# Optimization experiments

Hardware: AMD Instinct MI355X
Metric: run time of the kernel (lower is better)

The kernel has to match this reference:

```python
import jax, jax.numpy as jnp
import numpy as np

DT = 0.01
NJ = 7  # panda: 7 revolute joints, serial chain, fixed base
G_ACC = 9.81


def skew(v):
    x, y, z = v[..., 0], v[..., 1], v[..., 2]
    O = jnp.zeros_like(x)
    return jnp.stack([jnp.stack([O, -z, y], -1),
                      jnp.stack([z, O, -x], -1),
                      jnp.stack([-y, x, O], -1)], -2)


def rodrigues(axis, q):
    # axis [3], q [B] -> [B,3,3]
    K = skew(axis)
    K2 = K @ K
    s = jnp.sin(q)[:, None, None]
    c = jnp.cos(q)[:, None, None]
    return jnp.eye(3, dtype=q.dtype) + s * K + (1.0 - c) * K2


def xmot(E, r, v):
    # motion transform child<-parent; E [B,3,3], r [3], v [B,6] ([w;u] ordering)
    w, u = v[:, :3], v[:, 3:]
    wn = jnp.einsum('bij,bj->bi', E, w)
    un = jnp.einsum('bij,bj->bi', E, u - jnp.cross(jnp.broadcast_to(r, u.shape), w))
    return jnp.concatenate([wn, un], -1)


def crm(v, m):
    # motion cross product v x m
    w, u = v[:, :3], v[:, 3:]
    return jnp.concatenate([jnp.cross(w, m[:, :3]),
                            jnp.cross(w, m[:, 3:]) + jnp.cross(u, m[:, :3])], -1)


def crf(v, f):
    # force cross product v x* f
    w, u = v[:, :3], v[:, 3:]
    n, ff = f[:, :3], f[:, 3:]
    return jnp.concatenate([jnp.cross(w, n) + jnp.cross(u, ff), jnp.cross(w, ff)], -1)


def spatial_inertia(mass, com, inertia):
    # [NJ] / [NJ,3] / [NJ,3,3] -> [NJ,6,6] in [w;v] ordering
    cx = skew(com)
    m = mass[:, None, None]
    top = jnp.concatenate([inertia + m * (cx @ jnp.swapaxes(cx, -1, -2)), m * cx], -1)
    bot = jnp.concatenate([m * jnp.swapaxes(cx, -1, -2),
                           m * jnp.broadcast_to(jnp.eye(3, dtype=mass.dtype), cx.shape)], -1)
    return jnp.concatenate([top, bot], -2)


def aba(q, qd, tau, axes, R_fix, p_fix, mass, com, inertia):
    B = q.shape[0]
    I6 = spatial_inertia(mass, com, inertia)  # [NJ,6,6]
    E_l, S_l, v_l, c_l, IA_l, pA_l = [], [], [], [], [], []
    v_prev = None
    # pass 1: kinematics + bias terms
    for i in range(NJ):
        Rw = jnp.einsum('ij,bjk->bik', R_fix[i], rodrigues(axes[i], q[:, i]))
        E = jnp.swapaxes(Rw, -1, -2)  # parent->child rotation
        S = jnp.concatenate([axes[i], jnp.zeros(3, dtype=q.dtype)])  # [6]
        vJ = qd[:, i:i + 1] * S
        v_i = vJ if i == 0 else xmot(E, p_fix[i], v_prev) + vJ
        c_i = crm(v_i, vJ)
        Iv = jnp.einsum('ij,bj->bi', I6[i], v_i)
        pA_i = crf(v_i, Iv)
        E_l.append(E); S_l.append(S); v_l.append(v_i); c_l.append(c_i)
        IA_l.append(jnp.broadcast_to(I6[i], (B, 6, 6)))
        pA_l.append(pA_i)
        v_prev = v_i
    # pass 2: articulated inertia backward sweep
    U_l = [None] * NJ; d_l = [None] * NJ; uu_l = [None] * NJ
    for i in reversed(range(NJ)):
        S = S_l[i]; IA = IA_l[i]
        U = jnp.einsum('bij,j->bi', IA, S)
        d = jnp.einsum('bi,i->b', U, S)
        uu = tau[:, i] - jnp.einsum('bi,i->b', pA_l[i], S)
        U_l[i], d_l[i], uu_l[i] = U, d, uu
        if i > 0:
            Ia = IA - U[:, :, None] * U[:, None, :] / d[:, None, None]
            pa = pA_l[i] + jnp.einsum('bij,bj->bi', Ia, c_l[i]) + U * (uu / d)[:, None]
            E = E_l[i]; rX = skew(p_fix[i])
            Z = jnp.zeros_like(E)
            Xm = jnp.concatenate([jnp.concatenate([E, Z], -1),
                                  jnp.concatenate([-jnp.einsum('bij,jk->bik', E, rX), E], -1)], -2)
            IA_l[i - 1] = IA_l[i - 1] + jnp.einsum('bji,bjk,bkl->bil', Xm, Ia, Xm)
            fE = jnp.einsum('bji,bj->bi', E, pa[:, 3:])
            nP = jnp.einsum('bji,bj->bi', E, pa[:, :3]) + jnp.cross(jnp.broadcast_to(p_fix[i], fE.shape), fE)
            pA_l[i - 1] = pA_l[i - 1] + jnp.concatenate([nP, fE], -1)
    # pass 3: accelerations (base spatial accel = -gravity)
    a_prev = jnp.broadcast_to(jnp.array([0, 0, 0, 0, 0, G_ACC], dtype=q.dtype), (B, 6))
    qdd = []
    for i in range(NJ):
        ap = xmot(E_l[i], p_fix[i], a_prev) + c_l[i]
        qdd_i = (uu_l[i] - jnp.einsum('bi,bi->b', U_l[i], ap)) / d_l[i]
        a_prev = ap + qdd_i[:, None] * S_l[i]
        qdd.append(qdd_i)
    return jnp.stack(qdd, -1)  # [B,NJ]


def _rx(a):
    c, s = np.cos(a), np.sin(a)
    return np.array([[1, 0, 0], [0, c, -s], [0, s, c]], np.float32)


def setup_inputs() -> dict:
    key = jax.random.key(0)
    k1, k2 = jax.random.split(key)
    B = 262144
    x = 0.5 * jax.random.normal(k1, (B, 2 * NJ), dtype=jnp.float32)
    u = 5.0 * jax.random.normal(k2, (B, NJ), dtype=jnp.float32)
    angles = [0.0, -np.pi / 2, np.pi / 2, np.pi / 2, -np.pi / 2, np.pi / 2, np.pi / 2]
    R_fix = jnp.asarray(np.stack([_rx(a) for a in angles]).astype(np.float32))
    p_fix = jnp.asarray(np.array([[0, 0, 0.333], [0, 0, 0], [0, -0.316, 0], [0.0825, 0, 0],
                                  [-0.0825, 0.384, 0], [0, 0, 0], [0.088, 0, 0]], np.float32))
    axes = jnp.asarray(np.tile(np.array([0, 0, 1], np.float32), (NJ, 1)))
    mass = jnp.asarray(np.array([4.97, 0.65, 3.23, 3.59, 1.23, 1.67, 0.735], np.float32))
    com = jnp.asarray(np.array([[0.003, 0.002, -0.06], [-0.003, -0.028, 0.003], [0.027, 0.039, -0.066],
                                [-0.053, 0.104, 0.027], [-0.012, 0.041, -0.038], [0.06, -0.014, -0.011],
                                [0.01, -0.004, 0.061]], np.float32))
    diags = np.array([[0.7, 0.7, 0.01], [0.008, 0.028, 0.025], [0.037, 0.036, 0.011],
                      [0.026, 0.028, 0.031], [0.036, 0.036, 0.011], [0.002, 0.004, 0.005],
                      [0.012, 0.010, 0.005]], np.float32)
    inertia = jnp.asarray(np.stack([np.diag(v) for v in diags]).astype(np.float32))
    return {"x": x, "u": u, "axes": axes, "R_fix": R_fix, "p_fix": p_fix,
            "mass": mass, "com": com, "inertia": inertia}


def reference(x, u, axes, R_fix, p_fix, mass, com, inertia):
    q, v = x[:, :NJ], x[:, NJ:]
    a = aba(q, v, u, axes, R_fix, p_fix, mass, com, inertia)
    v_next = v + DT * a            # semi-implicit Euler
    q_next = q + DT * v_next
    return jnp.concatenate([q_next, v_next], -1)
```

## Files before the change

### kernel.cpp

```cpp
#include <hip/hip_runtime.h>

#define NJ 7
#define TB 64
static constexpr float DT_C    = 0.01f;
static constexpr float G_ACC_C = 9.81f;

static constexpr float RF[NJ][9] = {
    {1,0,0,  0,1,0,  0,0,1},
    {1,0,0,  0,0,1,  0,-1,0},
    {1,0,0,  0,0,-1, 0,1,0},
    {1,0,0,  0,0,-1, 0,1,0},
    {1,0,0,  0,0,1,  0,-1,0},
    {1,0,0,  0,0,-1, 0,1,0},
    {1,0,0,  0,0,-1, 0,1,0},
};
static constexpr float PFX[NJ][3] = {
    {0.f, 0.f, 0.333f},
    {0.f, 0.f, 0.f},
    {0.f, -0.316f, 0.f},
    {0.0825f, 0.f, 0.f},
    {-0.0825f, 0.384f, 0.f},
    {0.f, 0.f, 0.f},
    {0.088f, 0.f, 0.f},
};
static constexpr float MS[NJ] = {4.97f, 0.65f, 3.23f, 3.59f, 1.23f, 1.67f, 0.735f};
static constexpr float CM[NJ][3] = {
    {0.003f, 0.002f, -0.06f},
    {-0.003f, -0.028f, 0.003f},
    {0.027f, 0.039f, -0.066f},
    {-0.053f, 0.104f, 0.027f},
    {-0.012f, 0.041f, -0.038f},
    {0.06f, -0.014f, -0.011f},
    {0.01f, -0.004f, 0.061f},
};
static constexpr float ID[NJ][3] = {
    {0.7f, 0.7f, 0.01f},
    {0.008f, 0.028f, 0.025f},
    {0.037f, 0.036f, 0.011f},
    {0.026f, 0.028f, 0.031f},
    {0.036f, 0.036f, 0.011f},
    {0.002f, 0.004f, 0.005f},
    {0.012f, 0.01f, 0.005f},
};

#define MAKE_E(Rf, s, c)                                                     \
    float E00 = (Rf)[0]*(c) + (Rf)[1]*(s);                                   \
    float E01 = (Rf)[3]*(c) + (Rf)[4]*(s);                                   \
    float E02 = (Rf)[6]*(c) + (Rf)[7]*(s);                                   \
    float E10 = (Rf)[1]*(c) - (Rf)[0]*(s);                                   \
    float E11 = (Rf)[4]*(c) - (Rf)[3]*(s);                                   \
    float E12 = (Rf)[7]*(c) - (Rf)[6]*(s);                                   \
    float E20 = (Rf)[2];                                                     \
    float E21 = (Rf)[5];                                                     \
    float E22 = (Rf)[8];

extern "C" __global__ __launch_bounds__(TB)
void aba_step_kernel(const float* __restrict__ x, const float* __restrict__ u,
                     float* __restrict__ out, int B)
{
    __shared__ float vbuf[TB * 37];

    const int tid = threadIdx.x;
    const int b   = blockIdx.x * TB + tid;
    if (b >= B) return;
    const int xb = b * 14;
    float* vr = vbuf + tid * 37;

    float qr[NJ], qdr[NJ];
    #pragma unroll
    for (int i = 0; i < NJ; ++i) qr[i]  = x[xb + i];
    #pragma unroll
    for (int i = 0; i < NJ; ++i) qdr[i] = x[xb + 7 + i];

    float v0, v1, v2, v3, v4, v5;

    {
        v0 = 0.f; v1 = 0.f; v2 = qdr[0]; v3 = 0.f; v4 = 0.f; v5 = 0.f;
        vr[0] = v0; vr[1] = v1; vr[2] = v2; vr[3] = v3; vr[4] = v4; vr[5] = v5;
        #pragma unroll
        for (int i = 1; i < NJ; ++i) {
            float s, c;
            __sincosf(qr[i], &s, &c);
            MAKE_E(RF[i], s, c)
            const float px = PFX[i][0], py = PFX[i][1], pz = PFX[i][2];
            float t0 = v3 - (py*v2 - pz*v1);
            float t1 = v4 - (pz*v0 - px*v2);
            float t2 = v5 - (px*v1 - py*v0);
            float nw0 = E00*v0 + E01*v1 + E02*v2;
            float nw1 = E10*v0 + E11*v1 + E12*v2;
            float nw2 = E20*v0 + E21*v1 + E22*v2;
            float nu0 = E00*t0 + E01*t1 + E02*t2;
            float nu1 = E10*t0 + E11*t1 + E12*t2;
            float nu2 = E20*t0 + E21*t1 + E22*t2;
            v0 = nw0; v1 = nw1; v2 = nw2 + qdr[i];
            v3 = nu0; v4 = nu1; v5 = nu2;
            if (i < 6) {
                vr[6*i+0] = v0; vr[6*i+1] = v1; vr[6*i+2] = v2;
                vr[6*i+3] = v3; vr[6*i+4] = v4; vr[6*i+5] = v5;
            }
        }
    }

    float PA[6] = {0,0,0,0,0,0};
    float PB[9] = {0,0,0,0,0,0,0,0,0};
    float PC[6] = {0,0,0,0,0,0};
    float AC0=0.f, AC1=0.f, AC2=0.f, AC3=0.f, AC4=0.f, AC5=0.f;
    float u60, u61, u62, u63, u64, u65;

    #pragma unroll
    for (int ii = 0; ii < NJ; ++ii) {
        const int i = NJ - 1 - ii;
        const float qd = qdr[i];

        const float m  = MS[i];
        const float cx = CM[i][0], cy = CM[i][1], cz = CM[i][2];
        const float cc = cx*cx + cy*cy + cz*cz;
        const float J0 = ID[i][0] + m*(cc - cx*cx);
        const float J1 = -(m*cx*cy);
        const float J2 = -(m*cx*cz);
        const float J3 = ID[i][1] + m*(cc - cy*cy);
        const float J4 = -(m*cy*cz);
        const float J5 = ID[i][2] + m*(cc - cz*cz);

        float n0 = J0*v0 + J1*v1 + J2*v2 + m*(cy*v5 - cz*v4);
        float n1 = J1*v0 + J3*v1 + J4*v2 + m*(cz*v3 - cx*v5);
        float n2 = J2*v0 + J4*v1 + J5*v2 + m*(cx*v4 - cy*v3);
        float f0 = m*(v1*cz - v2*cy + v3);
        float f1 = m*(v2*cx - v0*cz + v4);
        float f2 = m*(v0*cy - v1*cx + v5);
        float p0 = v1*n2 - v2*n1 + v4*f2 - v5*f1 + AC0;
        float p1 = v2*n0 - v0*n2 + v5*f0 - v3*f2 + AC1;
        float p2 = v0*n1 - v1*n0 + v3*f1 - v4*f0 + AC2;
        float p3 = v1*f2 - v2*f1 + AC3;
        float p4 = v2*f0 - v0*f2 + AC4;
        float p5 = v0*f1 - v1*f0 + AC5;

        float A0 = J0 + PA[0]; float A1 = J1 + PA[1]; float A2 = J2 + PA[2];
        float A3 = J3 + PA[3]; float A4 = J4 + PA[4]; float A5 = J5 + PA[5];
        float B00 = PB[0];          float B01 = PB[1] - m*cz;  float B02 = PB[2] + m*cy;
        float B10 = PB[3] + m*cz;   float B11 = PB[4];         float B12 = PB[5] - m*cx;
        float B20 = PB[6] - m*cy;   float B21 = PB[7] + m*cx;  float B22 = PB[8];
        float C0 = PC[0] + m, C1 = PC[1],     C2 = PC[2];
        float C3 = PC[3] + m, C4 = PC[4],     C5 = PC[5] + m;

        float uu   = u[b*NJ + i] - p2;
        float invd = __builtin_amdgcn_rcpf(A5);
        float k    = uu * invd;
        float t0 = A2*invd, t1 = A4*invd;
        float t3 = B20*invd, t4 = B21*invd, t5 = B22*invd;

        if (i > 0) {
            float a00 = A0 - A2*t0, a01 = A1 - A2*t1, a11 = A3 - A4*t1;
            float b00 = B00 - A2*t3, b01 = B01 - A2*t4, b02 = B02 - A2*t5;
            float b10 = B10 - A4*t3, b11 = B11 - A4*t4, b12 = B12 - A4*t5;
            float c00 = C0 - B20*t3, c01 = C1 - B20*t4, c02 = C2 - B20*t5;
            float c11 = C3 - B21*t4, c12 = C4 - B21*t5, c22 = C5 - B22*t5;

            float q0 = v1*qd, q1 = -v0*qd, q3 = v4*qd, q4 = -v3*qd;
            float pa0 = p0 + a00*q0 + a01*q1 + b00*q3 + b01*q4 + A2*k;
            float pa1 = p1 + a01*q0 + a11*q1 + b10*q3 + b11*q4 + A4*k;
            float pa2 = p2 + uu;
            float pa3 = p3 + b00*q0 + b10*q1 + c00*q3 + c01*q4 + B20*k;
            float pa4 = p4 + b01*q0 + b11*q1 + c01*q3 + c11*q4 + B21*k;
            float pa5 = p5 + b02*q0 + b12*q1 + c02*q3 + c12*q4 + B22*k;

            float s, c;
            __sincosf(qr[i], &s, &c);
            MAKE_E(RF[i], s, c)
            const float px = PFX[i][0], py = PFX[i][1], pz = PFX[i][2];

            float fE0 = E00*pa3 + E10*pa4 + E20*pa5;
            float fE1 = E01*pa3 + E11*pa4 + E21*pa5;
            float fE2 = E02*pa3 + E12*pa4 + E22*pa5;
            AC0 = E00*pa0 + E10*pa1 + E20*pa2 + (py*fE2 - pz*fE1);
            AC1 = E01*pa0 + E11*pa1 + E21*pa2 + (pz*fE0 - px*fE2);
            AC2 = E02*pa0 + E12*pa1 + E22*pa2 + (px*fE1 - py*fE0);
            AC3 = fE0; AC4 = fE1; AC5 = fE2;

            float AE00 = a00*E00 + a01*E10, AE01 = a00*E01 + a01*E11, AE02 = a00*E02 + a01*E12;
            float AE10 = a01*E00 + a11*E10, AE11 = a01*E01 + a11*E11, AE12 = a01*E02 + a11*E12;
            float Ap00 = E00*AE00 + E10*AE10;
            float Ap01 = E00*AE01 + E10*AE11;
            float Ap02 = E00*AE02 + E10*AE12;
            float Ap11 = E01*AE01 + E11*AE11;
            float Ap12 = E01*AE02 + E11*AE12;
            float Ap22 = E02*AE02 + E12*AE12;
            float BE00 = b00*E00 + b01*E10 + b02*E20;
            float BE01 = b00*E01 + b01*E11 + b02*E21;
            float BE02 = b00*E02 + b01*E12 + b02*E22;
            float BE10 = b10*E00 + b11*E10 + b12*E20;
            float BE11 = b10*E01 + b11*E11 + b12*E21;
            float BE12 = b10*E02 + b11*E12 + b12*E22;
            float Bp00 = E00*BE00 + E10*BE10, Bp01 = E00*BE01 + E10*BE11, Bp02 = E00*BE02 + E10*BE12;
            float Bp10 = E01*BE00 + E11*BE10, Bp11 = E01*BE01 + E11*BE11, Bp12 = E01*BE02 + E11*BE12;
            float Bp20 = E02*BE00 + E12*BE10, Bp21 = E02*BE01 + E12*BE11, Bp22 = E02*BE02 + E12*BE12;
            float CE00 = c00*E00 + c01*E10 + c02*E20;
            float CE01 = c00*E01 + c01*E11 + c02*E21;
            float CE02 = c00*E02 + c01*E12 + c02*E22;
            float CE10 = c01*E00 + c11*E10 + c12*E20;
            float CE11 = c01*E01 + c11*E11 + c12*E21;
            float CE12 = c01*E02 + c11*E12 + c12*E22;
            float CE20 = c02*E00 + c12*E10 + c22*E20;
            float CE21 = c02*E01 + c12*E11 + c22*E21;
            float CE22 = c02*E02 + c12*E12 + c22*E22;
            float Cp00 = E00*CE00 + E10*CE10 + E20*CE20;
            float Cp01 = E00*CE01 + E10*CE11 + E20*CE21;
            float Cp02 = E00*CE02 + E10*CE12 + E20*CE22;
            float Cp11 = E01*CE01 + E11*CE11 + E21*CE21;
            float Cp12 = E01*CE02 + E11*CE12 + E21*CE22;
            float Cp22 = E02*CE02 + E12*CE12 + E22*CE22;
            float G00 = Bp01*pz - Bp02*py, G01 = Bp02*px - Bp00*pz, G02 = Bp00*py - Bp01*px;
            float G10 = Bp11*pz - Bp12*py, G11 = Bp12*px - Bp10*pz, G12 = Bp10*py - Bp11*px;
            float G20 = Bp21*pz - Bp22*py, G21 = Bp22*px - Bp20*pz, G22 = Bp20*py - Bp21*px;
            float H00 = Cp01*pz - Cp02*py, H01 = Cp02*px - Cp00*pz, H02 = Cp00*py - Cp01*px;
            float H10 = Cp11*pz - Cp12*py, H11 = Cp12*px - Cp01*pz, H12 = Cp01*py - Cp11*px;
            float H20 = Cp12*pz - Cp22*py, H21 = Cp22*px - Cp02*pz, H22 = Cp02*py - Cp12*px;
            float PH00 = py*H20 - pz*H10;
            float PH01 = py*H21 - pz*H11;
            float PH02 = py*H22 - pz*H12;
            float PH11 = pz*H01 - px*H21;
            float PH12 = pz*H02 - px*H22;
            float PH22 = px*H12 - py*H02;

            float nv0 = vr[6*(i-1)+0], nv1 = vr[6*(i-1)+1], nv2 = vr[6*(i-1)+2];
            float nv3 = vr[6*(i-1)+3], nv4 = vr[6*(i-1)+4], nv5 = vr[6*(i-1)+5];

            PA[0] = Ap00 - G00 - G00 - PH00;
            PA[1] = Ap01 - G01 - G10 - PH01;
            PA[2] = Ap02 - G02 - G20 - PH02;
            PA[3] = Ap11 - G11 - G11 - PH11;
            PA[4] = Ap12 - G12 - G21 - PH12;
            PA[5] = Ap22 - G22 - G22 - PH22;
            PB[0] = Bp00 + py*Cp02 - pz*Cp01;
            PB[1] = Bp01 + py*Cp12 - pz*Cp11;
            PB[2] = Bp02 + py*Cp22 - pz*Cp12;
            PB[3] = Bp10 + pz*Cp00 - px*Cp02;
            PB[4] = Bp11 + pz*Cp01 - px*Cp12;
            PB[5] = Bp12 + pz*Cp02 - px*Cp22;
            PB[6] = Bp20 + px*Cp01 - py*Cp00;
            PB[7] = Bp21 + px*Cp11 - py*Cp01;
            PB[8] = Bp22 + px*Cp12 - py*Cp02;
            PC[0] = Cp00; PC[1] = Cp01; PC[2] = Cp02;
            PC[3] = Cp11; PC[4] = Cp12; PC[5] = Cp22;

            v0 = nv0; v1 = nv1; v2 = nv2; v3 = nv3; v4 = nv4; v5 = nv5;
        }
        if (i == 6) {
            u60 = t0; u61 = t1; u62 = t3; u63 = t4; u64 = t5; u65 = k;
        } else {
            vr[6*i+0] = t0; vr[6*i+1] = t1; vr[6*i+2] = t3;
            vr[6*i+3] = t4; vr[6*i+4] = t5; vr[6*i+5] = k;
        }
    }

    {
        float a0=0.f, a1=0.f, a2=0.f, a3=0.f, a4=0.f, a5=G_ACC_C;
        float w0=0.f, w1=0.f, w2=0.f, w3=0.f, w4=0.f, w5=0.f;
        #pragma unroll
        for (int i = 0; i < NJ; ++i) {
            const float qd = qdr[i];
            float s, c;
            __sincosf(qr[i], &s, &c);
            MAKE_E(RF[i], s, c)
            const float px = PFX[i][0], py = PFX[i][1], pz = PFX[i][2];
            if (i == 0) {
                w2 = qd;
            } else {
                float r0 = w3 - (py*w2 - pz*w1);
                float r1 = w4 - (pz*w0 - px*w2);
                float r2 = w5 - (px*w1 - py*w0);
                float nw0 = E00*w0 + E01*w1 + E02*w2;
                float nw1 = E10*w0 + E11*w1 + E12*w2;
                float nw2 = E20*w0 + E21*w1 + E22*w2;
                float nu0 = E00*r0 + E01*r1 + E02*r2;
                float nu1 = E10*r0 + E11*r1 + E12*r2;
                float nu2 = E20*r0 + E21*r1 + E22*r2;
                w0 = nw0; w1 = nw1; w2 = nw2 + qd;
                w3 = nu0; w4 = nu1; w5 = nu2;
            }
            float cl0 = w1*qd, cl1 = -w0*qd, cl3 = w4*qd, cl4 = -w3*qd;
            float r0 = a3 - (py*a2 - pz*a1);
            float r1 = a4 - (pz*a0 - px*a2);
            float r2 = a5 - (px*a1 - py*a0);
            float ap0 = E00*a0 + E01*a1 + E02*a2 + cl0;
            float ap1 = E10*a0 + E11*a1 + E12*a2 + cl1;
            float ap2 = E20*a0 + E21*a1 + E22*a2;
            float ap3 = E00*r0 + E01*r1 + E02*r2 + cl3;
            float ap4 = E10*r0 + E11*r1 + E12*r2 + cl4;
            float ap5 = E20*r0 + E21*r1 + E22*r2;
            float d0, d1, d2, d3, d4, d5;
            if (i == 6) {
                d0 = u60; d1 = u61; d2 = u62; d3 = u63; d4 = u64; d5 = u65;
            } else {
                d0 = vr[6*i+0]; d1 = vr[6*i+1]; d2 = vr[6*i+2];
                d3 = vr[6*i+3]; d4 = vr[6*i+4]; d5 = vr[6*i+5];
            }
            float qdd = d5 - (d0*ap0 + d1*ap1 + ap2 + d2*ap3 + d3*ap4 + d4*ap5);
            a0 = ap0; a1 = ap1; a2 = ap2 + qdd;
            a3 = ap3; a4 = ap4; a5 = ap5;
            float vn = qd + DT_C*qdd;
            out[xb + 7 + i] = vn;
            out[xb + i]     = qr[i] + DT_C*vn;
        }
    }
}

extern "C" void kernel_launch(void* const* d_in, const int* in_sizes, int n_in,
                              void* d_out, int out_size, void* d_ws, size_t ws_size,
                              hipStream_t stream) {
    const float* x = (const float*)d_in[0];
    const float* u = (const float*)d_in[1];
    float* out = (float*)d_out;
    int B = in_sizes[0] / (2*NJ);
    int threads = TB;
    int blocks = (B + threads - 1) / threads;
    hipLaunchKernelGGL(aba_step_kernel, dim3(blocks), dim3(threads), 0, stream,
                       x, u, out, B);
}
```

Baseline: 112.4 us.

## Roll backward ABA pass into runtime loop with precomputed inertia constants

Changes the backward articulated-inertia pass from a fully unrolled loop to a rolled loop (unroll 1) over joints 6..1, peeling joint 0 into a reduced tail block. Per-link inertia terms (J, m*c) are precomputed as constexpr tables, and q/qd are reloaded from global memory instead of held in registers. Block size also grows from 64 to 256. The intent is to shrink code size and register pressure to raise occupancy. The cost is runtime indexing into the constant tables and vr array, which may force scratch memory or constant loads, plus redundant global reloads.

```diff
diff --git a/kernel.cpp b/kernel.cpp
--- a/kernel.cpp
+++ b/kernel.cpp
@@ -1,7 +1,7 @@
 #include <hip/hip_runtime.h>
 
 #define NJ 7
-#define TB 64
+#define TB 256
 static constexpr float DT_C    = 0.01f;
 static constexpr float G_ACC_C = 9.81f;
 
@@ -42,6 +42,27 @@
     {0.002f, 0.004f, 0.005f},
     {0.012f, 0.01f, 0.005f},
 };
+
+struct Derived {
+    float J[NJ][6];
+    float MC[NJ][3];
+};
+static constexpr Derived make_derived() {
+    Derived d{};
+    for (int i = 0; i < NJ; ++i) {
+        float m = MS[i], cx = CM[i][0], cy = CM[i][1], cz = CM[i][2];
+        float cc = cx*cx + cy*cy + cz*cz;
+        d.J[i][0] = ID[i][0] + m*(cc - cx*cx);
+        d.J[i][1] = -(m*cx*cy);
+        d.J[i][2] = -(m*cx*cz);
+        d.J[i][3] = ID[i][1] + m*(cc - cy*cy);
+        d.J[i][4] = -(m*cy*cz);
+        d.J[i][5] = ID[i][2] + m*(cc - cz*cz);
+        d.MC[i][0] = m*cx; d.MC[i][1] = m*cy; d.MC[i][2] = m*cz;
+    }
+    return d;
+}
+static constexpr Derived DRV = make_derived();
 
 #define MAKE_E(Rf, s, c)                                                     \
     float E00 = (Rf)[0]*(c) + (Rf)[1]*(s);                                   \
@@ -105,29 +126,22 @@
     float PB[9] = {0,0,0,0,0,0,0,0,0};
     float PC[6] = {0,0,0,0,0,0};
     float AC0=0.f, AC1=0.f, AC2=0.f, AC3=0.f, AC4=0.f, AC5=0.f;
-    float u60, u61, u62, u63, u64, u65;
-
-    #pragma unroll
-    for (int ii = 0; ii < NJ; ++ii) {
-        const int i = NJ - 1 - ii;
-        const float qd = qdr[i];
-
-        const float m  = MS[i];
-        const float cx = CM[i][0], cy = CM[i][1], cz = CM[i][2];
-        const float cc = cx*cx + cy*cy + cz*cz;
-        const float J0 = ID[i][0] + m*(cc - cx*cx);
-        const float J1 = -(m*cx*cy);
-        const float J2 = -(m*cx*cz);
-        const float J3 = ID[i][1] + m*(cc - cy*cy);
-        const float J4 = -(m*cy*cz);
-        const float J5 = ID[i][2] + m*(cc - cz*cz);
-
-        float n0 = J0*v0 + J1*v1 + J2*v2 + m*(cy*v5 - cz*v4);
-        float n1 = J1*v0 + J3*v1 + J4*v2 + m*(cz*v3 - cx*v5);
-        float n2 = J2*v0 + J4*v1 + J5*v2 + m*(cx*v4 - cy*v3);
-        float f0 = m*(v1*cz - v2*cy + v3);
-        float f1 = m*(v2*cx - v0*cz + v4);
-        float f2 = m*(v0*cy - v1*cx + v5);
+    float u60=0.f, u61=0.f, u62=0.f, u63=0.f, u64=0.f, u65=0.f;
+
+    #pragma unroll 1
+    for (int i = 6; i >= 1; --i) {
+        const float qd = x[xb + 7 + i];
+        const float m   = MS[i];
+        const float mcx = DRV.MC[i][0], mcy = DRV.MC[i][1], mcz = DRV.MC[i][2];
+        const float J0 = DRV.J[i][0], J1 = DRV.J[i][1], J2 = DRV.J[i][2];
+        const float J3 = DRV.J[i][3], J4 = DRV.J[i][4], J5 = DRV.J[i][5];
+
+        float n0 = J0*v0 + J1*v1 + J2*v2 + (mcy*v5 - mcz*v4);
+        float n1 = J1*v0 + J3*v1 + J4*v2 + (mcz*v3 - mcx*v5);
+        float n2 = J2*v0 + J4*v1 + J5*v2 + (mcx*v4 - mcy*v3);
+        float f0 = v1*mcz - v2*mcy + m*v3;
+        float f1 = v2*mcx - v0*mcz + m*v4;
+        float f2 = v0*mcy - v1*mcx + m*v5;
         float p0 = v1*n2 - v2*n1 + v4*f2 - v5*f1 + AC0;
         float p1 = v2*n0 - v0*n2 + v5*f0 - v3*f2 + AC1;
         float p2 = v0*n1 - v1*n0 + v3*f1 - v4*f0 + AC2;
@@ -137,9 +151,9 @@
 
         float A0 = J0 + PA[0]; float A1 = J1 + PA[1]; float A2 = J2 + PA[2];
         float A3 = J3 + PA[3]; float A4 = J4 + PA[4]; float A5 = J5 + PA[5];
-        float B00 = PB[0];          float B01 = PB[1] - m*cz;  float B02 = PB[2] + m*cy;
-        float B10 = PB[3] + m*cz;   float B11 = PB[4];         float B12 = PB[5] - m*cx;
-        float B20 = PB[6] - m*cy;   float B21 = PB[7] + m*cx;  float B22 = PB[8];
+        float B00 = PB[0];        float B01 = PB[1] - mcz;  float B02 = PB[2] + mcy;
+        float B10 = PB[3] + mcz;  float B11 = PB[4];        float B12 = PB[5] - mcx;
+        float B20 = PB[6] - mcy;  float B21 = PB[7] + mcx;  float B22 = PB[8];
         float C0 = PC[0] + m, C1 = PC[1],     C2 = PC[2];
         float C3 = PC[3] + m, C4 = PC[4],     C5 = PC[5] + m;
 
@@ -149,108 +163,135 @@
         float t0 = A2*invd, t1 = A4*invd;
         float t3 = B20*invd, t4 = B21*invd, t5 = B22*invd;
 
-        if (i > 0) {
-            float a00 = A0 - A2*t0, a01 = A1 - A2*t1, a11 = A3 - A4*t1;
-            float b00 = B00 - A2*t3, b01 = B01 - A2*t4, b02 = B02 - A2*t5;
-            float b10 = B10 - A4*t3, b11 = B11 - A4*t4, b12 = B12 - A4*t5;
-            float c00 = C0 - B20*t3, c01 = C1 - B20*t4, c02 = C2 - B20*t5;
-            float c11 = C3 - B21*t4, c12 = C4 - B21*t5, c22 = C5 - B22*t5;
-
-            float q0 = v1*qd, q1 = -v0*qd, q3 = v4*qd, q4 = -v3*qd;
-            float pa0 = p0 + a00*q0 + a01*q1 + b00*q3 + b01*q4 + A2*k;
-            float pa1 = p1 + a01*q0 + a11*q1 + b10*q3 + b11*q4 + A4*k;
-            float pa2 = p2 + uu;
-            float pa3 = p3 + b00*q0 + b10*q1 + c00*q3 + c01*q4 + B20*k;
-            float pa4 = p4 + b01*q0 + b11*q1 + c01*q3 + c11*q4 + B21*k;
-            float pa5 = p5 + b02*q0 + b12*q1 + c02*q3 + c12*q4 + B22*k;
-
-            float s, c;
-            __sincosf(qr[i], &s, &c);
-            MAKE_E(RF[i], s, c)
-            const float px = PFX[i][0], py = PFX[i][1], pz = PFX[i][2];
-
-            float fE0 = E00*pa3 + E10*pa4 + E20*pa5;
-            float fE1 = E01*pa3 + E11*pa4 + E21*pa5;
-            float fE2 = E02*pa3 + E12*pa4 + E22*pa5;
-            AC0 = E00*pa0 + E10*pa1 + E20*pa2 + (py*fE2 - pz*fE1);
-            AC1 = E01*pa0 + E11*pa1 + E21*pa2 + (pz*fE0 - px*fE2);
-            AC2 = E02*pa0 + E12*pa1 + E22*pa2 + (px*fE1 - py*fE0);
-            AC3 = fE0; AC4 = fE1; AC5 = fE2;
-
-            float AE00 = a00*E00 + a01*E10, AE01 = a00*E01 + a01*E11, AE02 = a00*E02 + a01*E12;
-            float AE10 = a01*E00 + a11*E10, AE11 = a01*E01 + a11*E11, AE12 = a01*E02 + a11*E12;
-            float Ap00 = E00*AE00 + E10*AE10;
-            float Ap01 = E00*AE01 + E10*AE11;
-            float Ap02 = E00*AE02 + E10*AE12;
-            float Ap11 = E01*AE01 + E11*AE11;
-            float Ap12 = E01*AE02 + E11*AE12;
-            float Ap22 = E02*AE02 + E12*AE12;
-            float BE00 = b00*E00 + b01*E10 + b02*E20;
-            float BE01 = b00*E01 + b01*E11 + b02*E21;
-            float BE02 = b00*E02 + b01*E12 + b02*E22;
-            float BE10 = b10*E00 + b11*E10 + b12*E20;
-            float BE11 = b10*E01 + b11*E11 + b12*E21;
-            float BE12 = b10*E02 + b11*E12 + b12*E22;
-            float Bp00 = E00*BE00 + E10*BE10, Bp01 = E00*BE01 + E10*BE11, Bp02 = E00*BE02 + E10*BE12;
-            float Bp10 = E01*BE00 + E11*BE10, Bp11 = E01*BE01 + E11*BE11, Bp12 = E01*BE02 + E11*BE12;
-            float Bp20 = E02*BE00 + E12*BE10, Bp21 = E02*BE01 + E12*BE11, Bp22 = E02*BE02 + E12*BE12;
-            float CE00 = c00*E00 + c01*E10 + c02*E20;
-            float CE01 = c00*E01 + c01*E11 + c02*E21;
-            float CE02 = c00*E02 + c01*E12 + c02*E22;
-            float CE10 = c01*E00 + c11*E10 + c12*E20;
-            float CE11 = c01*E01 + c11*E11 + c12*E21;
-            float CE12 = c01*E02 + c11*E12 + c12*E22;
-            float CE20 = c02*E00 + c12*E10 + c22*E20;
-            float CE21 = c02*E01 + c12*E11 + c22*E21;
-            float CE22 = c02*E02 + c12*E12 + c22*E22;
-            float Cp00 = E00*CE00 + E10*CE10 + E20*CE20;
-            float Cp01 = E00*CE01 + E10*CE11 + E20*CE21;
-            float Cp02 = E00*CE02 + E10*CE12 + E20*CE22;
-            float Cp11 = E01*CE01 + E11*CE11 + E21*CE21;
-            float Cp12 = E01*CE02 + E11*CE12 + E21*CE22;
-            float Cp22 = E02*CE02 + E12*CE12 + E22*CE22;
-            float G00 = Bp01*pz - Bp02*py, G01 = Bp02*px - Bp00*pz, G02 = Bp00*py - Bp01*px;
-            float G10 = Bp11*pz - Bp12*py, G11 = Bp12*px - Bp10*pz, G12 = Bp10*py - Bp11*px;
-            float G20 = Bp21*pz - Bp22*py, G21 = Bp22*px - Bp20*pz, G22 = Bp20*py - Bp21*px;
-            float H00 = Cp01*pz - Cp02*py, H01 = Cp02*px - Cp00*pz, H02 = Cp00*py - Cp01*px;
-            float H10 = Cp11*pz - Cp12*py, H11 = Cp12*px - Cp01*pz, H12 = Cp01*py - Cp11*px;
-            float H20 = Cp12*pz - Cp22*py, H21 = Cp22*px - Cp02*pz, H22 = Cp02*py - Cp12*px;
-            float PH00 = py*H20 - pz*H10;
-            float PH01 = py*H21 - pz*H11;
-            float PH02 = py*H22 - pz*H12;
-            float PH11 = pz*H01 - px*H21;
-            float PH12 = pz*H02 - px*H22;
-            float PH22 = px*H12 - py*H02;
-
-            float nv0 = vr[6*(i-1)+0], nv1 = vr[6*(i-1)+1], nv2 = vr[6*(i-1)+2];
-            float nv3 = vr[6*(i-1)+3], nv4 = vr[6*(i-1)+4], nv5 = vr[6*(i-1)+5];
-
-            PA[0] = Ap00 - G00 - G00 - PH00;
-            PA[1] = Ap01 - G01 - G10 - PH01;
-            PA[2] = Ap02 - G02 - G20 - PH02;
-            PA[3] = Ap11 - G11 - G11 - PH11;
-            PA[4] = Ap12 - G12 - G21 - PH12;
-            PA[5] = Ap22 - G22 - G22 - PH22;
-            PB[0] = Bp00 + py*Cp02 - pz*Cp01;
-            PB[1] = Bp01 + py*Cp12 - pz*Cp11;
-            PB[2] = Bp02 + py*Cp22 - pz*Cp12;
-            PB[3] = Bp10 + pz*Cp00 - px*Cp02;
-            PB[4] = Bp11 + pz*Cp01 - px*Cp12;
-            PB[5] = Bp12 + pz*Cp02 - px*Cp22;
-            PB[6] = Bp20 + px*Cp01 - py*Cp00;
-            PB[7] = Bp21 + px*Cp11 - py*Cp01;
-            PB[8] = Bp22 + px*Cp12 - py*Cp02;
-            PC[0] = Cp00; PC[1] = Cp01; PC[2] = Cp02;
-            PC[3] = Cp11; PC[4] = Cp12; PC[5] = Cp22;
-
-            v0 = nv0; v1 = nv1; v2 = nv2; v3 = nv3; v4 = nv4; v5 = nv5;
-        }
         if (i == 6) {
             u60 = t0; u61 = t1; u62 = t3; u63 = t4; u64 = t5; u65 = k;
         } else {
             vr[6*i+0] = t0; vr[6*i+1] = t1; vr[6*i+2] = t3;
             vr[6*i+3] = t4; vr[6*i+4] = t5; vr[6*i+5] = k;
         }
+
+        float a00 = A0 - A2*t0, a01 = A1 - A2*t1, a11 = A3 - A4*t1;
+        float b00 = B00 - A2*t3, b01 = B01 - A2*t4, b02 = B02 - A2*t5;
+        float b10 = B10 - A4*t3, b11 = B11 - A4*t4, b12 = B12 - A4*t5;
+        float c00 = C0 - B20*t3, c01 = C1 - B20*t4, c02 = C2 - B20*t5;
+        float c11 = C3 - B21*t4, c12 = C4 - B21*t5, c22 = C5 - B22*t5;
+
+        float q0 = v1*qd, q1 = -v0*qd, q3 = v4*qd, q4 = -v3*qd;
+        float pa0 = p0 + a00*q0 + a01*q1 + b00*q3 + b01*q4 + A2*k;
+        float pa1 = p1 + a01*q0 + a11*q1 + b10*q3 + b11*q4 + A4*k;
+        float pa2 = p2 + uu;
+        float pa3 = p3 + b00*q0 + b10*q1 + c00*q3 + c01*q4 + B20*k;
+        float pa4 = p4 + b01*q0 + b11*q1 + c01*q3 + c11*q4 + B21*k;
+        float pa5 = p5 + b02*q0 + b12*q1 + c02*q3 + c12*q4 + B22*k;
+
+        float s, c;
+        __sincosf(x[xb + i], &s, &c);
+        const float R0 = RF[i][0], R1 = RF[i][1], R3 = RF[i][3],
+                    R4 = RF[i][4], R6 = RF[i][6], R7 = RF[i][7];
+        float E00 = R0*c + R1*s, E01 = R3*c + R4*s, E02 = R6*c + R7*s;
+        float E10 = R1*c - R0*s, E11 = R4*c - R3*s, E12 = R7*c - R6*s;
+        const float E20 = RF[i][2], E21 = RF[i][5], E22 = RF[i][8];
+        const float px = PFX[i][0], py = PFX[i][1], pz = PFX[i][2];
+
+        float fE0 = E00*pa3 + E10*pa4 + E20*pa5;
+        float fE1 = E01*pa3 + E11*pa4 + E21*pa5;
+        float fE2 = E02*pa3 + E12*pa4 + E22*pa5;
+        AC0 = E00*pa0 + E10*pa1 + E20*pa2 + (py*fE2 - pz*fE1);
+        AC1 = E01*pa0 + E11*pa1 + E21*pa2 + (pz*fE0 - px*fE2);
+        AC2 = E02*pa0 + E12*pa1 + E22*pa2 + (px*fE1 - py*fE0);
+        AC3 = fE0; AC4 = fE1; AC5 = fE2;
+
+        float AE00 = a00*E00 + a01*E10, AE01 = a00*E01 + a01*E11, AE02 = a00*E02 + a01*E12;
+        float AE10 = a01*E00 + a11*E10, AE11 = a01*E01 + a11*E11, AE12 = a01*E02 + a11*E12;
+        float Ap00 = E00*AE00 + E10*AE10;
+        float Ap01 = E00*AE01 + E10*AE11;
+        float Ap02 = E00*AE02 + E10*AE12;
+        float Ap11 = E01*AE01 + E11*AE11;
+        float Ap12 = E01*AE02 + E11*AE12;
+        float Ap22 = E02*AE02 + E12*AE12;
+        float BE00 = b00*E00 + b01*E10 + b02*E20;
+        float BE01 = b00*E01 + b01*E11 + b02*E21;
+        float BE02 = b00*E02 + b01*E12 + b02*E22;
+        float BE10 = b10*E00 + b11*E10 + b12*E20;
+        float BE11 = b10*E01 + b11*E11 + b12*E21;
+        float BE12 = b10*E02 + b11*E12 + b12*E22;
+        float Bp00 = E00*BE00 + E10*BE10, Bp01 = E00*BE01 + E10*BE11, Bp02 = E00*BE02 + E10*BE12;
+        float Bp10 = E01*BE00 + E11*BE10, Bp11 = E01*BE01 + E11*BE11, Bp12 = E01*BE02 + E11*BE12;
+        float Bp20 = E02*BE00 + E12*BE10, Bp21 = E02*BE01 + E12*BE11, Bp22 = E02*BE02 + E12*BE12;
+        float CE00 = c00*E00 + c01*E10 + c02*E20;
+        float CE01 = c00*E01 + c01*E11 + c02*E21;
+        float CE02 = c00*E02 + c01*E12 + c02*E22;
+        float CE10 = c01*E00 + c11*E10 + c12*E20;
+        float CE11 = c01*E01 + c11*E11 + c12*E21;
+        float CE12 = c01*E02 + c11*E12 + c12*E22;
+        float CE20 = c02*E00 + c12*E10 + c22*E20;
+        float CE21 = c02*E01 + c12*E11 + c22*E21;
+        float CE22 = c02*E02 + c12*E12 + c22*E22;
+        float Cp00 = E00*CE00 + E10*CE10 + E20*CE20;
+        float Cp01 = E00*CE01 + E10*CE11 + E20*CE21;
+        float Cp02 = E00*CE02 + E10*CE12 + E20*CE22;
+        float Cp11 = E01*CE01 + E11*CE11 + E21*CE21;
+        float Cp12 = E01*CE02 + E11*CE12 + E21*CE22;
+        float Cp22 = E02*CE02 + E12*CE12 + E22*CE22;
+        float G00 = Bp01*pz - Bp02*py, G01 = Bp02*px - Bp00*pz, G02 = Bp00*py - Bp01*px;
+        float G10 = Bp11*pz - Bp12*py, G11 = Bp12*px - Bp10*pz, G12 = Bp10*py - Bp11*px;
+        float G20 = Bp21*pz - Bp22*py, G21 = Bp22*px - Bp20*pz, G22 = Bp20*py - Bp21*px;
+        float H00 = Cp01*pz - Cp02*py, H01 = Cp02*px - Cp00*pz, H02 = Cp00*py - Cp01*px;
+        float H10 = Cp11*pz - Cp12*py, H11 = Cp12*px - Cp01*pz, H12 = Cp01*py - Cp11*px;
+        float H20 = Cp12*pz - Cp22*py, H21 = Cp22*px - Cp02*pz, H22 = Cp02*py - Cp12*px;
+        float PH00 = py*H20 - pz*H10;
+        float PH01 = py*H21 - pz*H11;
+        float PH02 = py*H22 - pz*H12;
+        float PH11 = pz*H01 - px*H21;
+        float PH12 = pz*H02 - px*H22;
+        float PH22 = px*H12 - py*H02;
+
+        float nv0 = vr[6*(i-1)+0], nv1 = vr[6*(i-1)+1], nv2 = vr[6*(i-1)+2];
+        float nv3 = vr[6*(i-1)+3], nv4 = vr[6*(i-1)+4], nv5 = vr[6*(i-1)+5];
+
+        PA[0] = Ap00 - G00 - G00 - PH00;
+        PA[1] = Ap01 - G01 - G10 - PH01;
+        PA[2] = Ap02 - G02 - G20 - PH02;
+        PA[3] = Ap11 - G11 - G11 - PH11;
+        PA[4] = Ap12 - G12 - G21 - PH12;
+        PA[5] = Ap22 - G22 - G22 - PH22;
+        PB[0] = Bp00 + py*Cp02 - pz*Cp01;
+        PB[1] = Bp01 + py*Cp12 - pz*Cp11;
+        PB[2] = Bp02 + py*Cp22 - pz*Cp12;
+        PB[3] = Bp10 + pz*Cp00 - px*Cp02;
+        PB[4] = Bp11 + pz*Cp01 - px*Cp12;
+        PB[5] = Bp12 + pz*Cp02 - px*Cp22;
+        PB[6] = Bp20 + px*Cp01 - py*Cp00;
+        PB[7] = Bp21 + px*Cp11 - py*Cp01;
+        PB[8] = Bp22 + px*Cp12 - py*Cp02;
+        PC[0] = Cp00; PC[1] = Cp01; PC[2] = Cp02;
+        PC[3] = Cp11; PC[4] = Cp12; PC[5] = Cp22;
+
+        v0 = nv0; v1 = nv1; v2 = nv2; v3 = nv3; v4 = nv4; v5 = nv5;
+    }
+
+    {
+        const float m   = MS[0];
+        const float mcx = DRV.MC[0][0], mcy = DRV.MC[0][1], mcz = DRV.MC[0][2];
+        const float J0 = DRV.J[0][0], J1 = DRV.J[0][1], J2 = DRV.J[0][2];
+        const float J3 = DRV.J[0][3], J4 = DRV.J[0][4], J5 = DRV.J[0][5];
+        float n0 = J0*v0 + J1*v1 + J2*v2 + (mcy*v5 - mcz*v4);
+        float n1 = J1*v0 + J3*v1 + J4*v2 + (mcz*v3 - mcx*v5);
+        float n2 = J2*v0 + J4*v1 + J5*v2 + (mcx*v4 - mcy*v3);
+        float f0 = v1*mcz - v2*mcy + m*v3;
+        float f1 = v2*mcx - v0*mcz + m*v4;
+        float f2 = v0*mcy - v1*mcx + m*v5;
+        float p2 = v0*n1 - v1*n0 + v3*f1 - v4*f0 + AC2;
+        float A2 = J2 + PA[2];
+        float A4 = J4 + PA[4];
+        float A5 = J5 + PA[5];
+        float B20 = PB[6] - mcy;  float B21 = PB[7] + mcx;  float B22 = PB[8];
+        float uu   = u[b*NJ + 0] - p2;
+        float invd = __builtin_amdgcn_rcpf(A5);
+        float k    = uu * invd;
+        vr[0] = A2*invd; vr[1] = A4*invd; vr[2] = B20*invd;
+        vr[3] = B21*invd; vr[4] = B22*invd; vr[5] = k;
+        (void)n2; (void)f2;
     }
 
     {
```

Result: faster. 108.1 us (-3.8%).
